# Kernel optimization log

Hardware: AMD Instinct MI355X
Metric: run time of the kernel (lower is better)

Reference implementation:

```python
import jax, jax.numpy as jnp
import numpy as np

# Camera intrinsics hardcoded in the original module
FX = 582.6244816773795
FY = 582.6910327098864
CX = 313.0447587080473
CY = 238.44389626620386
S = 7            # sample_size
P = (S - 1) // 2  # padding_size = 3


def setup_inputs() -> dict:
    key = jax.random.key(0)
    k1, k2 = jax.random.split(key)
    depthin = jax.random.uniform(k1, (1, 1, 480, 640), dtype=jnp.float32)
    gt = jax.random.uniform(k2, (1, 1, 480, 640), dtype=jnp.float32)
    return {"depthin": depthin, "gt": gt}


def _stdev_loss(depthin):
    depth = depthin[0, 0]
    rows, cols = depth.shape
    c = jnp.arange(cols, dtype=depth.dtype)            # [cols]
    r = jnp.arange(rows, dtype=depth.dtype)[:, None]   # [rows,1]
    valid = (depth > 0) & (depth < 1.01)
    zero = jnp.zeros((), depth.dtype)
    z = jnp.where(valid, depth / 1000.0, zero)
    x = jnp.where(valid, z * (c - CX) / FX, zero)
    y = jnp.where(valid, z * (r - CY) / FY, zero)

    # Clamped window start: istart = clip(i - P, 0, rows - S) reproduces the
    # idif/jdif boundary-shift logic of the original nested loop exactly.
    ii = jnp.clip(jnp.arange(rows) - P, 0, rows - S)[:, None] + jnp.arange(S)  # [rows,S]
    jj = jnp.clip(jnp.arange(cols) - P, 0, cols - S)[:, None] + jnp.arange(S)  # [cols,S]

    def patches(a):
        # gather 7x7 clamped windows for every pixel -> [rows, cols, S, S]
        return a[ii[:, None, :, None], jj[None, :, None, :]]

    dist = jnp.sqrt(
        (x[:, :, None, None] - patches(x)) ** 2
        + (y[:, :, None, None] - patches(y)) ** 2
        + (z[:, :, None, None] - patches(z)) ** 2
    )  # [rows, cols, S, S]
    d = dist.reshape(rows, cols, S * S)
    mean = d.mean(axis=-1, keepdims=True)
    # torch.std default: unbiased (Bessel-corrected, n-1)
    var = jnp.sum((d - mean) ** 2, axis=-1) / (S * S - 1)
    dev = jnp.where(valid, jnp.sqrt(var), zero)
    return dev.sum() * 100.0


def reference(depthin, gt):
    # NOTE: the original also adds DDDDepthDiff()(depthin, gt); that class is
    # not defined in the provided source, so the reference covers the windowed
    # 3D-point-distance std term (the hot path) only. gt is accepted but unused.
    return _stdev_loss(depthin)
```

## Files before the change

kernel.cpp:

```cpp
#include <hip/hip_runtime.h>
#include <math.h>

static constexpr int ROWS = 480;
static constexpr int COLS = 640;
static constexpr int S = 7;
static constexpr int P = 3;
static constexpr int BX = 16, BY = 16;
static constexpr int TW = BX + 2 * P;
static constexpr int TP = 24;

__global__ void zero_out_kernel(float* out) { out[0] = 0.0f; }

__global__ __launch_bounds__(BX * BY)
void stdev_loss_kernel(const float* __restrict__ depth, float* __restrict__ out) {
    __shared__ float sx[TW][TP];
    __shared__ float sy[TW][TP];
    __shared__ float sz[TW][TP];

    const int tx = threadIdx.x, ty = threadIdx.y;
    const int bx0 = blockIdx.x * BX;
    const int by0 = blockIdx.y * BY;
    const int tid = ty * BX + tx;

    const float CXc = 313.0447587080473f;
    const float CYc = 238.44389626620386f;
    const float RFX = (float)(1.0 / 582.6244816773795);
    const float RFY = (float)(1.0 / 582.6910327098864);

    for (int t = tid; t < TW * TW; t += BX * BY) {
        const int lr = t / TW, lc = t % TW;
        int gr = by0 + lr - P; gr = min(max(gr, 0), ROWS - 1);
        int gc = bx0 + lc - P; gc = min(max(gc, 0), COLS - 1);
        const float d = depth[gr * COLS + gc];
        const bool v = (d > 0.0f) && (d < 1.01f);
        const float z = v ? d * 1.0e-3f : 0.0f;
        sx[lr][lc] = v ? z * ((float)gc - CXc) * RFX : 0.0f;
        sy[lr][lc] = v ? z * ((float)gr - CYc) * RFY : 0.0f;
        sz[lr][lc] = z;
    }
    __syncthreads();

    const int gi = by0 + ty;
    const int gj = bx0 + tx;
    const int is = min(max(gi - P, 0), ROWS - S) - by0 + P;
    const int js = min(max(gj - P, 0), COLS - S) - bx0 + P;

    const float vx = sx[ty + P][tx + P];
    const float vy = sy[ty + P][tx + P];
    const float vz = sz[ty + P][tx + P];

    float sum = 0.0f, sumsq = 0.0f;
#pragma unroll
    for (int a = 0; a < S; ++a) {
#pragma unroll
        for (int b = 0; b < S; ++b) {
            const float dx = vx - sx[is + a][js + b];
            const float dy = vy - sy[is + a][js + b];
            const float dz = vz - sz[is + a][js + b];
            const float t = dx * dx + dy * dy + dz * dz;
            sumsq += t;
            sum   += sqrtf(t);
        }
    }
    const float mean = sum * (1.0f / 49.0f);
    float var = (sumsq - sum * mean) * (1.0f / 48.0f);
    var = fmaxf(var, 0.0f);
    float dev = (vz > 0.0f) ? sqrtf(var) : 0.0f;

    float r = dev;
#pragma unroll
    for (int off = 32; off > 0; off >>= 1) r += __shfl_down(r, off, 64);

    __shared__ float red[(BX * BY) / 64];
    const int lane = tid & 63, wave = tid >> 6;
    if (lane == 0) red[wave] = r;
    __syncthreads();
    if (tid == 0) {
        float bsum = 0.0f;
#pragma unroll
        for (int w = 0; w < (BX * BY) / 64; ++w) bsum += red[w];
        atomicAdd(out, bsum * 100.0f);
    }
}

extern "C" void kernel_launch(void* const* d_in, const int* in_sizes, int n_in,
                              void* d_out, int out_size, void* d_ws, size_t ws_size,
                              hipStream_t stream) {
    const float* depth = (const float*)d_in[0];
    float* out = (float*)d_out;

    zero_out_kernel<<<1, 1, 0, stream>>>(out);
    dim3 block(BX, BY);
    dim3 grid(COLS / BX, ROWS / BY);
    stdev_loss_kernel<<<grid, block, 0, stream>>>(depth, out);
}
```

Measured before the change: 75.83 us.

## Compute two vertically adjacent pixels per thread sharing window row loads

```diff
diff --git a/kernel.cpp b/kernel.cpp
--- a/kernel.cpp
+++ b/kernel.cpp
@@ -6,20 +6,21 @@
 static constexpr int S = 7;
 static constexpr int P = 3;
 static constexpr int BX = 16, BY = 16;
-static constexpr int TW = BX + 2 * P;
+static constexpr int PXY = 2;
+static constexpr int TILE_H = BY * PXY;
+static constexpr int TW_X = BX + 2 * P;
+static constexpr int TW_Y = TILE_H + 2 * P;
 static constexpr int TP = 24;
-
-__global__ void zero_out_kernel(float* out) { out[0] = 0.0f; }
 
 __global__ __launch_bounds__(BX * BY)
 void stdev_loss_kernel(const float* __restrict__ depth, float* __restrict__ out) {
-    __shared__ float sx[TW][TP];
-    __shared__ float sy[TW][TP];
-    __shared__ float sz[TW][TP];
+    __shared__ float sx[TW_Y][TP];
+    __shared__ float sy[TW_Y][TP];
+    __shared__ float sz[TW_Y][TP];
 
     const int tx = threadIdx.x, ty = threadIdx.y;
     const int bx0 = blockIdx.x * BX;
-    const int by0 = blockIdx.y * BY;
+    const int by0 = blockIdx.y * TILE_H;
     const int tid = ty * BX + tx;
 
     const float CXc = 313.0447587080473f;
@@ -27,10 +28,10 @@
     const float RFX = (float)(1.0 / 582.6244816773795);
     const float RFY = (float)(1.0 / 582.6910327098864);
 
-    for (int t = tid; t < TW * TW; t += BX * BY) {
-        const int lr = t / TW, lc = t % TW;
-        int gr = by0 + lr - P; gr = min(max(gr, 0), ROWS - 1);
-        int gc = bx0 + lc - P; gc = min(max(gc, 0), COLS - 1);
+    for (int t = tid; t < TW_Y * TW_X; t += BX * BY) {
+        const int lr = t / TW_X, lc = t % TW_X;
+        int gr = min(max(by0 + lr - P, 0), ROWS - 1);
+        int gc = min(max(bx0 + lc - P, 0), COLS - 1);
         const float d = depth[gr * COLS + gc];
         const bool v = (d > 0.0f) && (d < 1.01f);
         const float z = v ? d * 1.0e-3f : 0.0f;
@@ -40,34 +41,60 @@
     }
     __syncthreads();
 
-    const int gi = by0 + ty;
-    const int gj = bx0 + tx;
-    const int is = min(max(gi - P, 0), ROWS - S) - by0 + P;
-    const int js = min(max(gj - P, 0), COLS - S) - bx0 + P;
+    const int gj  = bx0 + tx;
+    const int gi0 = by0 + PXY * ty;
+    const int jsl  = min(max(gj - P, 0), COLS - S) - bx0 + P;
+    const int is0g = min(max(gi0 - P, 0), ROWS - S);
+    const int is1g = min(max(gi0 + 1 - P, 0), ROWS - S);
+    const int is0l = is0g - by0 + P;
+    const float g_first = (is1g == is0g) ? 1.0f : 0.0f;
+    const float g_last  = 1.0f - g_first;
 
-    const float vx = sx[ty + P][tx + P];
-    const float vy = sy[ty + P][tx + P];
-    const float vz = sz[ty + P][tx + P];
+    const int cr0 = PXY * ty + P, cc = tx + P;
+    const float vx0 = sx[cr0][cc],     vy0 = sy[cr0][cc],     vz0 = sz[cr0][cc];
+    const float vx1 = sx[cr0 + 1][cc], vy1 = sy[cr0 + 1][cc], vz1 = sz[cr0 + 1][cc];
 
-    float sum = 0.0f, sumsq = 0.0f;
+    float sum0 = 0.0f, sq0 = 0.0f, sum1 = 0.0f, sq1 = 0.0f;
 #pragma unroll
-    for (int a = 0; a < S; ++a) {
+    for (int a = 0; a < S + 1; ++a) {
+        const int r = is0l + a;
+        float nx[S], ny[S], nz[S];
 #pragma unroll
         for (int b = 0; b < S; ++b) {
-            const float dx = vx - sx[is + a][js + b];
-            const float dy = vy - sy[is + a][js + b];
-            const float dz = vz - sz[is + a][js + b];
+            nx[b] = sx[r][jsl + b];
+            ny[b] = sy[r][jsl + b];
+            nz[b] = sz[r][jsl + b];
+        }
+        if (a < S) {
+#pragma unroll
+            for (int b = 0; b < S; ++b) {
+                const float dx = vx0 - nx[b], dy = vy0 - ny[b], dz = vz0 - nz[b];
+                const float t = dx * dx + dy * dy + dz * dz;
+                sq0 += t;
+                sum0 += __builtin_amdgcn_sqrtf(t);
+            }
+        }
+        float rs = 0.0f, rq = 0.0f;
+#pragma unroll
+        for (int b = 0; b < S; ++b) {
+            const float dx = vx1 - nx[b], dy = vy1 - ny[b], dz = vz1 - nz[b];
             const float t = dx * dx + dy * dy + dz * dz;
-            sumsq += t;
-            sum   += sqrtf(t);
+            rq += t;
+            rs += __builtin_amdgcn_sqrtf(t);
         }
+        if (a == 0)      { sum1 += g_first * rs; sq1 += g_first * rq; }
+        else if (a == S) { sum1 += g_last * rs;  sq1 += g_last * rq; }
+        else             { sum1 += rs;           sq1 += rq; }
     }
-    const float mean = sum * (1.0f / 49.0f);
-    float var = (sumsq - sum * mean) * (1.0f / 48.0f);
-    var = fmaxf(var, 0.0f);
-    float dev = (vz > 0.0f) ? sqrtf(var) : 0.0f;
 
-    float r = dev;
+    const float mean0 = sum0 * (1.0f / 49.0f);
+    float var0 = fmaxf((sq0 - sum0 * mean0) * (1.0f / 48.0f), 0.0f);
+    const float dev0 = (vz0 > 0.0f) ? __builtin_amdgcn_sqrtf(var0) : 0.0f;
+    const float mean1 = sum1 * (1.0f / 49.0f);
+    float var1 = fmaxf((sq1 - sum1 * mean1) * (1.0f / 48.0f), 0.0f);
+    const float dev1 = (vz1 > 0.0f) ? __builtin_amdgcn_sqrtf(var1) : 0.0f;
+
+    float r = dev0 + dev1;
 #pragma unroll
     for (int off = 32; off > 0; off >>= 1) r += __shfl_down(r, off, 64);
 
@@ -89,8 +116,8 @@
     const float* depth = (const float*)d_in[0];
     float* out = (float*)d_out;
 
-    zero_out_kernel<<<1, 1, 0, stream>>>(out);
+    hipMemsetAsync(out, 0, sizeof(float), stream);
     dim3 block(BX, BY);
-    dim3 grid(COLS / BX, ROWS / BY);
+    dim3 grid(COLS / BX, ROWS / TILE_H);
     stdev_loss_kernel<<<grid, block, 0, stream>>>(depth, out);
 }
```

After: 68.28 us. 10.0% less time.
